# Kernel tuning notes

Hardware: AMD Instinct MI355X
Metric: run time of the kernel (lower is better)

## Reference

```python
import jax, jax.numpy as jnp
import numpy as np

P = 256          # patches per (batch*time) element
EPS = 1e-6
WEIGHT_SIM = 1.0
WEIGHT_GRAM = 10.0


def setup_inputs() -> dict:
    key = jax.random.key(0)
    k1, k2 = jax.random.split(key)
    N, D = 16384, 768  # N = bt * P with bt = 64
    inp = jax.random.normal(k1, (N, D), dtype=jnp.float32)
    tgt = jax.random.normal(k2, (N, D), dtype=jnp.float32)
    return {"input": inp, "target": tgt}


def _l2n(x):
    return x / jnp.sqrt(jnp.sum(x * x, axis=-1, keepdims=True)).clip(1e-12)


def reference(input, target):
    target = jax.lax.stop_gradient(target)
    N, D = input.shape
    bt = N // P

    input_n = _l2n(input)
    target_n = _l2n(target)

    input_view = input.reshape(bt, P, D)
    target_view = target.reshape(bt, P, D)
    in_n = input_n.reshape(bt, P, D)
    tg_n = target_n.reshape(bt, P, D)

    # gram of normalized targets; its row-mean gives tf
    gram_gt = jnp.einsum('bpd,bqd->bpq', tg_n, tg_n)           # [bt, P, P]
    tf = 1.0 / (gram_gt.mean(axis=-1) + EPS)                    # [bt, P]

    # cross_sim.mean(dim=-1) == all_patches @ mean(all_patches): O(N*d) not O(N^2*d)
    mean_patch = target_n.mean(axis=0)                          # [D]
    cross_mean = target_n @ mean_patch                          # [N]
    idf = 1.0 / (cross_mean.reshape(bt, P) + EPS)               # [bt, P]

    weights = tf * idf
    weights = weights / (weights.sum(axis=1, keepdims=True) + EPS)

    patch_loss = jnp.mean((input_view - target_view) ** 2, axis=-1)  # [bt, P]
    sim_loss = jnp.mean(jnp.sum(weights * patch_loss, axis=1))

    gram_pred = jnp.einsum('bpd,bqd->bpq', in_n, in_n)          # [bt, P, P]
    diff2 = (gram_pred - gram_gt) ** 2
    pair_w = weights[:, :, None] * weights[:, None, :]          # [bt, P, P]
    gram_loss = jnp.mean(jnp.sum(pair_w * diff2, axis=(1, 2)))

    return WEIGHT_SIM * sim_loss + WEIGHT_GRAM * gram_loss
```

## Files before the change

kernel.cpp:

```cpp
#include <hip/hip_runtime.h>
#include <hip/hip_bf16.h>

#define NROWS 16384
#define DIM   768
#define PP    256
#define BT    64
#define EPSF  1e-6f
#define GKC   32
#define NTILE 10
#define NGRAM (BT * NTILE)
#define SPITCH 776
#define RPW    4
#define NWG_N  (NROWS / RPW)

typedef short          bf16x8 __attribute__((ext_vector_type(8)));
typedef float          f32x4  __attribute__((ext_vector_type(4)));
typedef unsigned short us8    __attribute__((ext_vector_type(8)));

__device__ __forceinline__ unsigned short f2bf(float x) {
    __hip_bfloat16 h = __float2bfloat16(x);
    return *reinterpret_cast<unsigned short*>(&h);
}

__global__ __launch_bounds__(256, 8) void k_norms(const float* __restrict__ in,
                                                  const float* __restrict__ tg,
                                                  float* __restrict__ inv_in,
                                                  float* __restrict__ inv_tg,
                                                  float* __restrict__ ploss,
                                                  float* __restrict__ psum) {
    __shared__ __align__(16) float S[RPW][SPITCH];
    const int r   = threadIdx.x >> 6;
    const int c   = threadIdx.x & 63;
    const int row = blockIdx.x * RPW + r;
    const float4* ip = (const float4*)(in + (size_t)row * DIM);
    const float4* tp = (const float4*)(tg + (size_t)row * DIM);
    float4 a[3], t[3];
#pragma unroll
    for (int k = 0; k < 3; ++k) { a[k] = ip[c + 64 * k]; t[k] = tp[c + 64 * k]; }
    float si = 0.f, st = 0.f, sd = 0.f;
#pragma unroll
    for (int k = 0; k < 3; ++k) {
        si += a[k].x*a[k].x + a[k].y*a[k].y + a[k].z*a[k].z + a[k].w*a[k].w;
        st += t[k].x*t[k].x + t[k].y*t[k].y + t[k].z*t[k].z + t[k].w*t[k].w;
        float dx = a[k].x-t[k].x, dy = a[k].y-t[k].y, dz = a[k].z-t[k].z, dw = a[k].w-t[k].w;
        sd += dx*dx + dy*dy + dz*dz + dw*dw;
    }
#pragma unroll
    for (int o = 32; o; o >>= 1) {
        si += __shfl_xor(si, o); st += __shfl_xor(st, o); sd += __shfl_xor(sd, o);
    }
    float ii = 1.f / fmaxf(sqrtf(si), 1e-12f);
    float it = 1.f / fmaxf(sqrtf(st), 1e-12f);
    if (c == 0) { inv_in[row] = ii; inv_tg[row] = it; ploss[row] = sd * (1.f / DIM); }

#pragma unroll
    for (int k = 0; k < 3; ++k) {
        float4 u = t[k];
        u.x *= it; u.y *= it; u.z *= it; u.w *= it;
        *(float4*)&S[r][4 * c + 256 * k] = u;
    }
    __syncthreads();
#pragma unroll
    for (int q = 0; q < 3; ++q) {
        int d = threadIdx.x + 256 * q;
        float s = 0.f;
#pragma unroll
        for (int rr = 0; rr < RPW; ++rr) s += S[rr][d];
        psum[(size_t)blockIdx.x * DIM + d] = s;
    }
}


__global__ __launch_bounds__(256) void k_bsum2(const float* __restrict__ psum,
                                               float* __restrict__ bsum) {
    int b = blockIdx.x, d = blockIdx.y * 256 + threadIdx.x;
    float s = 0.f;
#pragma unroll 8
    for (int i = 0; i < 64; ++i)
        s += psum[(size_t)(b * 64 + i) * DIM + d];
    bsum[b * DIM + d] = s;
}

__global__ __launch_bounds__(256) void k_gmean(const float* __restrict__ bsum,
                                               float* __restrict__ va) {
    int d = blockIdx.x * 256 + threadIdx.x;
    float g = 0.f;
    for (int b = 0; b < BT; ++b) g += bsum[b * DIM + d];
    va[d] = g * (1.f / NROWS);
}

__global__ __launch_bounds__(256) void k_wdots(const float* __restrict__ tg,
                                               const float* __restrict__ inv_tg,
                                               const float* __restrict__ bsum,
                                               const float* __restrict__ va,
                                               float* __restrict__ wraw) {
    int wave = threadIdx.x >> 6, lane = threadIdx.x & 63;
    int gw = blockIdx.x * 4 + wave;
#pragma unroll
    for (int rr = 0; rr < 4; ++rr) {
        int row = gw * 4 + rr;
        int b   = row >> 8;
        const float4* t4 = (const float4*)(tg + (size_t)row * DIM);
        const float4* b4 = (const float4*)(bsum + b * DIM);
        const float4* a4 = (const float4*)va;
        float db = 0.f, da = 0.f;
#pragma unroll
        for (int v = 0; v < 3; ++v) {
            float4 t = t4[lane + 64 * v];
            float4 x = b4[lane + 64 * v];
            float4 y = a4[lane + 64 * v];
            db += t.x * x.x + t.y * x.y + t.z * x.z + t.w * x.w;
            da += t.x * y.x + t.y * y.y + t.z * y.z + t.w * y.w;
        }
#pragma unroll
        for (int o = 32; o; o >>= 1) { db += __shfl_xor(db, o); da += __shfl_xor(da, o); }
        if (lane == 0) {
            float itg = inv_tg[row];
            db *= itg; da *= itg;
            wraw[row] = (1.f / (db * (1.f / PP) + EPSF)) * (1.f / (da + EPSF));
        }
    }
}

__global__ __launch_bounds__(256) void k_wfinal(const float* __restrict__ wraw,
                                                const float* __restrict__ ploss,
                                                float* __restrict__ weights,
                                                float* __restrict__ simpart) {
    __shared__ float red[256];
    int b = blockIdx.x, p = threadIdx.x, row = b * PP + p;
    float w = wraw[row];
    red[p] = w; __syncthreads();
    for (int s = 128; s; s >>= 1) { if (p < s) red[p] += red[p + s]; __syncthreads(); }
    float wn = w / (red[0] + EPSF);
    weights[row] = wn;
    __syncthreads();
    red[p] = wn * ploss[row]; __syncthreads();
    for (int s = 128; s; s >>= 1) { if (p < s) red[p] += red[p + s]; __syncthreads(); }
    if (p == 0) simpart[b] = red[0];
}

__global__ __launch_bounds__(256, 3) void k_gram(const float* __restrict__ in,
                                                 const float* __restrict__ tg,
                                                 const float* __restrict__ inv_in,
                                                 const float* __restrict__ inv_tg,
                                                 const float* __restrict__ weights,
                                                 float* __restrict__ grampart) {
    __shared__ __align__(16) unsigned short L[2][4][64 * GKC];
    __shared__ float red[256];

    const int wg  = blockIdx.x;
    const int xcd = wg & 7, j = wg >> 3;
    const int b   = xcd * 8 + j / NTILE;
    const int t   = j % NTILE;
    int ti, tj;
    if (t < 4)      { ti = 0; tj = t; }
    else if (t < 7) { ti = 1; tj = t - 3; }
    else if (t < 9) { ti = 2; tj = t - 5; }
    else            { ti = 3; tj = 3; }
    const int pr = ti * 64, qc = tj * 64;
    const bool diag = (ti == tj);
    const float factor = diag ? 1.f : 2.f;
    const int bP = b * PP;

    const int tid = threadIdx.x, lane = tid & 63, wave = tid >> 6;

    const float* smat = (wave & 1) ? tg : in;
    const int  srow0   = bP + ((wave < 2) ? pr : qc);
    const bool doStage = !(diag && wave >= 2);
    const int  srl = lane >> 2;
    const int  scc = lane & 3;
    const int  wcc = scc ^ (srl & 3);

    float4 p0[4], p1[4];
    auto LD = [&](int k0) {
        if (!doStage) return;
#pragma unroll
        for (int i = 0; i < 4; ++i) {
            const float* base = smat + (size_t)(srow0 + 16 * i + srl) * DIM + k0 + scc * 8;
            p0[i] = *(const float4*)base;
            p1[i] = *(const float4*)(base + 4);
        }
    };
    auto WR = [&](int cur) {
        if (!doStage) return;
#pragma unroll
        for (int i = 0; i < 4; ++i) {
            us8 v;
            v[0] = f2bf(p0[i].x); v[1] = f2bf(p0[i].y);
            v[2] = f2bf(p0[i].z); v[3] = f2bf(p0[i].w);
            v[4] = f2bf(p1[i].x); v[5] = f2bf(p1[i].y);
            v[6] = f2bf(p1[i].z); v[7] = f2bf(p1[i].w);
            *(us8*)&L[cur][wave][(16 * i + srl) * GKC + wcc * 8] = v;
        }
    };

    const int ar0 = (wave >> 1) * 32, bc0 = (wave & 1) * 32;
    const int rl = lane & 15, kc = lane >> 4;
    const int bi_ = diag ? 0 : 2, bt_ = diag ? 1 : 3;

    f32x4 accI[2][2], accT[2][2];
#pragma unroll
    for (int m = 0; m < 2; ++m)
#pragma unroll
        for (int n = 0; n < 2; ++n) {
            f32x4 z = { 0.f, 0.f, 0.f, 0.f };
            accI[m][n] = z; accT[m][n] = z;
        }

    LD(0); WR(0);
    int cur = 0;
    const int NS = DIM / GKC;
    for (int ks = 0; ks < NS; ++ks) {
        if (ks + 1 < NS) LD((ks + 1) * GKC);
        __syncthreads();
        bf16x8 aI[2], aT[2], bI[2], bT[2];
#pragma unroll
        for (int m = 0; m < 2; ++m) {
            int row = ar0 + m * 16 + rl;
            int off = row * GKC + ((kc ^ (row & 3)) << 3);
            aI[m] = *(const bf16x8*)&L[cur][0][off];
            aT[m] = *(const bf16x8*)&L[cur][1][off];
        }
#pragma unroll
        for (int n = 0; n < 2; ++n) {
            int row = bc0 + n * 16 + rl;
            int off = row * GKC + ((kc ^ (row & 3)) << 3);
            bI[n] = *(const bf16x8*)&L[cur][bi_][off];
            bT[n] = *(const bf16x8*)&L[cur][bt_][off];
        }
#pragma unroll
        for (int m = 0; m < 2; ++m)
#pragma unroll
            for (int n = 0; n < 2; ++n) {
                accI[m][n] = __builtin_amdgcn_mfma_f32_16x16x32_bf16(aI[m], bI[n], accI[m][n], 0, 0, 0);
                accT[m][n] = __builtin_amdgcn_mfma_f32_16x16x32_bf16(aT[m], bT[n], accT[m][n], 0, 0, 0);
            }
        if (ks + 1 < NS) WR(cur ^ 1);
        cur ^= 1;
    }

    const int r4 = lane >> 4, cl = lane & 15;
    float wq[2], qI[2], qT[2];
#pragma unroll
    for (int n = 0; n < 2; ++n) {
        int q = bP + qc + bc0 + n * 16 + cl;
        wq[n] = weights[q]; qI[n] = inv_in[q]; qT[n] = inv_tg[q];
    }
    float wp[2][4], pI[2][4], pT[2][4];
#pragma unroll
    for (int m = 0; m < 2; ++m)
#pragma unroll
        for (int r = 0; r < 4; ++r) {
            int p = bP + pr + ar0 + m * 16 + r4 * 4 + r;
            wp[m][r] = weights[p]; pI[m][r] = inv_in[p]; pT[m][r] = inv_tg[p];
        }
    float local = 0.f;
#pragma unroll
    for (int m = 0; m < 2; ++m)
#pragma unroll
        for (int n = 0; n < 2; ++n)
#pragma unroll
            for (int r = 0; r < 4; ++r) {
                float d = accI[m][n][r] * pI[m][r] * qI[n]
                        - accT[m][n][r] * pT[m][r] * qT[n];
                local += wp[m][r] * wq[n] * d * d;
            }
    local *= factor;
    red[tid] = local; __syncthreads();
    for (int s = 128; s; s >>= 1) { if (tid < s) red[tid] += red[tid + s]; __syncthreads(); }
    if (tid == 0) grampart[wg] = red[0];
}

__global__ __launch_bounds__(256) void k_final(const float* __restrict__ simpart,
                                               const float* __restrict__ grampart,
                                               int ngram,
                                               float* __restrict__ out) {
    __shared__ float red[256];
    int t = threadIdx.x;
    float v = (t < BT) ? simpart[t] : 0.f;
    float g = 0.f;
    for (int i = t; i < ngram; i += 256) g += grampart[i];
    v += 10.f * g;
    red[t] = v; __syncthreads();
    for (int s = 128; s; s >>= 1) { if (t < s) red[t] += red[t + s]; __syncthreads(); }
    if (t == 0) out[0] = red[0] * (1.f / BT);
}

extern "C" void kernel_launch(void* const* d_in, const int* in_sizes, int n_in,
                              void* d_out, int out_size, void* d_ws, size_t ws_size,
                              hipStream_t stream) {
    (void)in_sizes; (void)n_in; (void)out_size; (void)ws_size;
    const float* in = (const float*)d_in[0];
    const float* tg = (const float*)d_in[1];

    float* fbase   = (float*)d_ws;
    float* inv_in  = fbase;
    float* inv_tg  = fbase + NROWS;
    float* ploss   = fbase + 2 * (size_t)NROWS;
    float* wraw    = fbase + 3 * (size_t)NROWS;
    float* weights = fbase + 4 * (size_t)NROWS;
    float* psum    = fbase + 5 * (size_t)NROWS;
    float* bsum    = psum + (size_t)NWG_N * DIM;
    float* va      = bsum + (size_t)BT * DIM;
    float* simpart = va + DIM;
    float* grampart= simpart + BT;

    k_norms<<<NWG_N, 256, 0, stream>>>(in, tg, inv_in, inv_tg, ploss, psum);
    k_bsum2<<<dim3(BT, 3), 256, 0, stream>>>(psum, bsum);
    k_gmean<<<3, 256, 0, stream>>>(bsum, va);
    k_wdots<<<NROWS / 16, 256, 0, stream>>>(tg, inv_tg, bsum, va, wraw);
    k_wfinal<<<BT, 256, 0, stream>>>(wraw, ploss, weights, simpart);
    k_gram<<<NGRAM, 256, 0, stream>>>(in, tg, inv_in, inv_tg, weights, grampart);
    k_final<<<1, 256, 0, stream>>>(simpart, grampart, NGRAM, (float*)d_out);
}
```

Baseline: 72.30 us.

## Pre-quantize normalized rows to FP8 and run gram tiles with FP8 MFMA

```diff
diff --git a/kernel.cpp b/kernel.cpp
--- a/kernel.cpp
+++ b/kernel.cpp
@@ -12,6 +12,8 @@
 #define SPITCH 776
 #define RPW    4
 #define NWG_N  (NROWS / RPW)
+#define F8SCALE 32.0f
+#define F8INV   (1.0f / 1024.0f)
 
 typedef short          bf16x8 __attribute__((ext_vector_type(8)));
 typedef float          f32x4  __attribute__((ext_vector_type(4)));
@@ -22,11 +24,20 @@
     return *reinterpret_cast<unsigned short*>(&h);
 }
 
+__device__ __forceinline__ unsigned int pk_fp8x4(float a, float b, float c, float d) {
+    int w = __builtin_amdgcn_cvt_pk_fp8_f32(a, b, 0, false);
+    w = __builtin_amdgcn_cvt_pk_fp8_f32(c, d, w, true);
+    return (unsigned int)w;
+}
+
+template<int PRE>
 __global__ __launch_bounds__(256, 8) void k_norms(const float* __restrict__ in,
                                                   const float* __restrict__ tg,
                                                   float* __restrict__ inv_in,
                                                   float* __restrict__ inv_tg,
                                                   float* __restrict__ ploss,
+                                                  unsigned char* __restrict__ in8,
+                                                  unsigned char* __restrict__ tg8,
                                                   float* __restrict__ psum) {
     __shared__ __align__(16) float S[RPW][SPITCH];
     const int r   = threadIdx.x >> 6;
@@ -59,6 +70,18 @@
         u.x *= it; u.y *= it; u.z *= it; u.w *= it;
         *(float4*)&S[r][4 * c + 256 * k] = u;
     }
+
+    if constexpr (PRE != 0) {
+        float is = ii * F8SCALE, ts = it * F8SCALE;
+#pragma unroll
+        for (int k = 0; k < 3; ++k) {
+            unsigned int wa = pk_fp8x4(a[k].x * is, a[k].y * is, a[k].z * is, a[k].w * is);
+            unsigned int wt = pk_fp8x4(t[k].x * ts, t[k].y * ts, t[k].z * ts, t[k].w * ts);
+            *(unsigned int*)(in8 + (size_t)row * DIM + 4 * c + 256 * k) = wa;
+            *(unsigned int*)(tg8 + (size_t)row * DIM + 4 * c + 256 * k) = wt;
+        }
+    }
+
     __syncthreads();
 #pragma unroll
     for (int q = 0; q < 3; ++q) {
@@ -139,13 +162,11 @@
     if (p == 0) simpart[b] = red[0];
 }
 
-__global__ __launch_bounds__(256, 3) void k_gram(const float* __restrict__ in,
-                                                 const float* __restrict__ tg,
-                                                 const float* __restrict__ inv_in,
-                                                 const float* __restrict__ inv_tg,
+__global__ __launch_bounds__(256, 4) void k_gram(const unsigned char* __restrict__ in8,
+                                                 const unsigned char* __restrict__ tg8,
                                                  const float* __restrict__ weights,
                                                  float* __restrict__ grampart) {
-    __shared__ __align__(16) unsigned short L[2][4][64 * GKC];
+    __shared__ __align__(16) unsigned char L[2][4][64 * GKC];
     __shared__ float red[256];
 
     const int wg  = blockIdx.x;
@@ -164,6 +185,121 @@
 
     const int tid = threadIdx.x, lane = tid & 63, wave = tid >> 6;
 
+    const unsigned char* smat = (wave & 1) ? tg8 : in8;
+    const int  srow0   = bP + ((wave < 2) ? pr : qc);
+    const bool doStage = !(diag && wave >= 2);
+    const int  srl = lane >> 2;
+    const int  scc = lane & 3;
+    const int  wcc = scc ^ (srl & 3);
+
+    unsigned long long sreg[4];
+    auto LD = [&](int k0) {
+        if (!doStage) return;
+#pragma unroll
+        for (int i = 0; i < 4; ++i)
+            sreg[i] = *(const unsigned long long*)(smat + (size_t)(srow0 + 16 * i + srl) * DIM + k0 + scc * 8);
+    };
+    auto WR = [&](int cur) {
+        if (!doStage) return;
+#pragma unroll
+        for (int i = 0; i < 4; ++i)
+            *(unsigned long long*)&L[cur][wave][(16 * i + srl) * GKC + wcc * 8] = sreg[i];
+    };
+
+    const int ar0 = (wave >> 1) * 32, bc0 = (wave & 1) * 32;
+    const int rl = lane & 15, kc = lane >> 4;
+    const int bi_ = diag ? 0 : 2, bt_ = diag ? 1 : 3;
+
+    f32x4 accI[2][2], accT[2][2];
+#pragma unroll
+    for (int m = 0; m < 2; ++m)
+#pragma unroll
+        for (int n = 0; n < 2; ++n) {
+            f32x4 z = { 0.f, 0.f, 0.f, 0.f };
+            accI[m][n] = z; accT[m][n] = z;
+        }
+
+    LD(0); WR(0);
+    int cur = 0;
+    const int NS = DIM / GKC;
+    for (int ks = 0; ks < NS; ++ks) {
+        if (ks + 1 < NS) LD((ks + 1) * GKC);
+        __syncthreads();
+        long long aI[2], aT[2], bI[2], bT[2];
+#pragma unroll
+        for (int m = 0; m < 2; ++m) {
+            int row = ar0 + m * 16 + rl;
+            int off = row * GKC + ((kc ^ (row & 3)) << 3);
+            aI[m] = *(const long long*)&L[cur][0][off];
+            aT[m] = *(const long long*)&L[cur][1][off];
+        }
+#pragma unroll
+        for (int n = 0; n < 2; ++n) {
+            int row = bc0 + n * 16 + rl;
+            int off = row * GKC + ((kc ^ (row & 3)) << 3);
+            bI[n] = *(const long long*)&L[cur][bi_][off];
+            bT[n] = *(const long long*)&L[cur][bt_][off];
+        }
+#pragma unroll
+        for (int m = 0; m < 2; ++m)
+#pragma unroll
+            for (int n = 0; n < 2; ++n) {
+                accI[m][n] = __builtin_amdgcn_mfma_f32_16x16x32_fp8_fp8(aI[m], bI[n], accI[m][n], 0, 0, 0);
+                accT[m][n] = __builtin_amdgcn_mfma_f32_16x16x32_fp8_fp8(aT[m], bT[n], accT[m][n], 0, 0, 0);
+            }
+        if (ks + 1 < NS) WR(cur ^ 1);
+        cur ^= 1;
+    }
+
+    const int r4 = lane >> 4, cl = lane & 15;
+    float wq[2], wp[2][4];
+#pragma unroll
+    for (int n = 0; n < 2; ++n) wq[n] = weights[bP + qc + bc0 + n * 16 + cl];
+#pragma unroll
+    for (int m = 0; m < 2; ++m)
+#pragma unroll
+        for (int r = 0; r < 4; ++r) wp[m][r] = weights[bP + pr + ar0 + m * 16 + r4 * 4 + r];
+    float local = 0.f;
+#pragma unroll
+    for (int m = 0; m < 2; ++m)
+#pragma unroll
+        for (int n = 0; n < 2; ++n)
+#pragma unroll
+            for (int r = 0; r < 4; ++r) {
+                float d = (accI[m][n][r] - accT[m][n][r]) * F8INV;
+                local += wp[m][r] * wq[n] * d * d;
+            }
+    local *= factor;
+    red[tid] = local; __syncthreads();
+    for (int s = 128; s; s >>= 1) { if (tid < s) red[tid] += red[tid + s]; __syncthreads(); }
+    if (tid == 0) grampart[wg] = red[0];
+}
+
+__global__ __launch_bounds__(256, 3) void k_gram_f32(const float* __restrict__ in,
+                                                     const float* __restrict__ tg,
+                                                     const float* __restrict__ inv_in,
+                                                     const float* __restrict__ inv_tg,
+                                                     const float* __restrict__ weights,
+                                                     float* __restrict__ grampart) {
+    __shared__ __align__(16) unsigned short L[2][4][64 * GKC];
+    __shared__ float red[256];
+
+    const int wg  = blockIdx.x;
+    const int xcd = wg & 7, j = wg >> 3;
+    const int b   = xcd * 8 + j / NTILE;
+    const int t   = j % NTILE;
+    int ti, tj;
+    if (t < 4)      { ti = 0; tj = t; }
+    else if (t < 7) { ti = 1; tj = t - 3; }
+    else if (t < 9) { ti = 2; tj = t - 5; }
+    else            { ti = 3; tj = 3; }
+    const int pr = ti * 64, qc = tj * 64;
+    const bool diag = (ti == tj);
+    const float factor = diag ? 1.f : 2.f;
+    const int bP = b * PP;
+
+    const int tid = threadIdx.x, lane = tid & 63, wave = tid >> 6;
+
     const float* smat = (wave & 1) ? tg : in;
     const int  srow0   = bP + ((wave < 2) ? pr : qc);
     const bool doStage = !(diag && wave >= 2);
@@ -289,11 +425,28 @@
 extern "C" void kernel_launch(void* const* d_in, const int* in_sizes, int n_in,
                               void* d_out, int out_size, void* d_ws, size_t ws_size,
                               hipStream_t stream) {
-    (void)in_sizes; (void)n_in; (void)out_size; (void)ws_size;
+    (void)in_sizes; (void)n_in; (void)out_size;
     const float* in = (const float*)d_in[0];
     const float* tg = (const float*)d_in[1];
 
-    float* fbase   = (float*)d_ws;
+    const size_t f8Bytes   = (size_t)NROWS * DIM;
+    const size_t floatsOff = 2 * f8Bytes;
+    const size_t fCount    = 5 * (size_t)NROWS + (size_t)NWG_N * DIM
+                           + (size_t)BT * DIM + DIM + BT + NGRAM;
+    const size_t needed    = floatsOff + fCount * 4;
+    const bool   pre       = ws_size >= needed;
+
+    char* wsb = (char*)d_ws;
+    unsigned char* in8 = nullptr;
+    unsigned char* tg8 = nullptr;
+    float* fbase;
+    if (pre) {
+        in8   = (unsigned char*)wsb;
+        tg8   = (unsigned char*)(wsb + f8Bytes);
+        fbase = (float*)(wsb + floatsOff);
+    } else {
+        fbase = (float*)wsb;
+    }
     float* inv_in  = fbase;
     float* inv_tg  = fbase + NROWS;
     float* ploss   = fbase + 2 * (size_t)NROWS;
@@ -305,11 +458,19 @@
     float* simpart = va + DIM;
     float* grampart= simpart + BT;
 
-    k_norms<<<NWG_N, 256, 0, stream>>>(in, tg, inv_in, inv_tg, ploss, psum);
+    if (pre) {
+        k_norms<1><<<NWG_N, 256, 0, stream>>>(in, tg, inv_in, inv_tg, ploss, in8, tg8, psum);
+    } else {
+        k_norms<0><<<NWG_N, 256, 0, stream>>>(in, tg, inv_in, inv_tg, ploss, nullptr, nullptr, psum);
+    }
     k_bsum2<<<dim3(BT, 3), 256, 0, stream>>>(psum, bsum);
     k_gmean<<<3, 256, 0, stream>>>(bsum, va);
     k_wdots<<<NROWS / 16, 256, 0, stream>>>(tg, inv_tg, bsum, va, wraw);
     k_wfinal<<<BT, 256, 0, stream>>>(wraw, ploss, weights, simpart);
-    k_gram<<<NGRAM, 256, 0, stream>>>(in, tg, inv_in, inv_tg, weights, grampart);
+    if (pre) {
+        k_gram<<<NGRAM, 256, 0, stream>>>(in8, tg8, weights, grampart);
+    } else {
+        k_gram_f32<<<NGRAM, 256, 0, stream>>>(in, tg, inv_in, inv_tg, weights, grampart);
+    }
     k_final<<<1, 256, 0, stream>>>(simpart, grampart, NGRAM, (float*)d_out);
 }
```

New measurement: 70.31 us. -2.8%, faster.
